# Performance work log

Measured on AMD Instinct MI355X. Metric: run time of the kernel, lower is better.

The kernel has to match this reference:

```python
import jax, jax.numpy as jnp
import numpy as np

EPS = 1e-7  # K.epsilon()


def setup_inputs() -> dict:
    key = jax.random.key(0)
    k1, k2, k3, k4, k5, k6 = jax.random.split(key, 6)
    B, S, D = 128, 1024, 256
    ATT, QDIM = 128, 128
    inp = {
        "key": jax.random.normal(k1, (B, S, D), dtype=jnp.float32),
        "query": jax.random.normal(k2, (QDIM, 1), dtype=jnp.float32),
        "mask": jax.random.randint(k3, (B, S), 0, 2, dtype=jnp.int32),
        # learned params (keras 'normal' init ~ N(0, 0.05))
        "W": 0.05 * jax.random.normal(k4, (D, ATT), dtype=jnp.float32),
        "b": 0.05 * jax.random.normal(k5, (ATT,), dtype=jnp.float32),
        "W_u": 0.05 * jax.random.normal(k6, (ATT, QDIM), dtype=jnp.float32),
    }
    return inp


def reference(key, query, mask, W, b, W_u):
    # uit = tanh(key @ W + b): (B,S,ATT)
    uit = jnp.tanh(jnp.einsum("bsd,da->bsa", key, W) + b)
    # u = W_u @ query: (ATT,1)
    u = W_u @ query
    # scores: (B,S)
    ait = jnp.einsum("bsa,a->bs", uit, u[:, 0])
    ait = jnp.exp(ait)
    ait = ait * mask.astype(jnp.float32)
    ait = ait / (jnp.sum(ait, axis=1, keepdims=True) + EPS)
    # weighted sum over sequence -> (B,D); value == key
    out = jnp.einsum("bs,bsd->bd", ait, key)
    return out
```

## Files before the change

### kernel.cpp

```cpp
#include <hip/hip_runtime.h>
#include <hip/hip_bf16.h>
#include <math.h>

#define EPS_F 1e-7f

constexpr int Bn = 128, Sn = 1024, Dn = 256, ATTn = 128, QDn = 128;
constexpr int Mn = Bn * Sn;
constexpr int BM = 128;
constexpr int NBLK = Mn / BM;
constexpr int KSTEPS = Dn / 32;
constexpr int NJ = ATTn / 16;

typedef short short8 __attribute__((ext_vector_type(8)));
typedef float f32x4  __attribute__((ext_vector_type(4)));

__device__ inline void split_bf(float f, ushort& hi, ushort& lo) {
    uint fb = __float_as_uint(f);
    hi = (ushort)(fb >> 16);
    float hf = __uint_as_float(fb & 0xffff0000u);
    float lf = f - hf;
    __hip_bfloat16 lb = __float2bfloat16(lf);
    __builtin_memcpy(&lo, &lb, 2);
}

__device__ inline float tanh_fast(float x) {
    float cx = fminf(9.0f, fmaxf(-9.0f, x));
    float e = __builtin_amdgcn_exp2f(cx * 2.8853900817779268f);
    return (e - 1.0f) * __builtin_amdgcn_rcpf(e + 1.0f);
}

__device__ inline void gload_lds16(const float* g, void* lds_base) {
    __builtin_amdgcn_global_load_lds(
        (const __attribute__((address_space(1))) unsigned int*)g,
        (__attribute__((address_space(3))) unsigned int*)lds_base, 16, 0, 0);
}


__global__ __launch_bounds__(256) void k_prep(
    const float* __restrict__ Wu, const float* __restrict__ q,
    float* __restrict__ u,
    const float* __restrict__ W,
    ushort* __restrict__ Bhi, ushort* __restrict__ Blo)
{
    if (blockIdx.x == 0) {
        __shared__ float qs[QDn];
        int t = threadIdx.x;
        if (t < QDn) qs[t] = q[t];
        __syncthreads();
        if (t < ATTn) {
            float acc = 0.f;
            #pragma unroll 8
            for (int j = 0; j < QDn; ++j) acc += Wu[t * QDn + j] * qs[j];
            u[t] = acc;
        }
        return;
    }
    int gid  = (blockIdx.x - 1) * 256 + threadIdx.x;
    int lane = gid & 63;
    int j    = (gid >> 6) & 7;
    int ks   = gid >> 9;
    int col  = j * 16 + (lane & 15);
    int kb   = ks * 32 + (lane >> 4) * 8;
    #pragma unroll
    for (int i = 0; i < 8; ++i) {
        float f = W[(size_t)(kb + i) * ATTn + col];
        ushort h, l;
        split_bf(f, h, l);
        size_t idx = (size_t)gid * 8 + i;
        Bhi[idx] = h; Blo[idx] = l;
    }
}

__global__ __launch_bounds__(256, 4) void k_scores(
    const float*  __restrict__ key,
    const ushort* __restrict__ Bhi, const ushort* __restrict__ Blo,
    const float*  __restrict__ bias, const float* __restrict__ u,
    const int*    __restrict__ mask,
    float* __restrict__ P, float* __restrict__ den)
{
    __shared__ float4 Atile[2][BM * 8];
    __shared__ float  es[BM];
    __shared__ float4 part[4][64];

    const int t    = threadIdx.x;
    const int lane = t & 63;
    const int w    = t >> 6;
    const int gb   = blockIdx.x;
    const int row0 = gb * BM;
    const int l15  = lane & 15;
    const int lg   = lane >> 4;

    const float* gsrc[4];
    int sbase[4];
    #pragma unroll
    for (int i = 0; i < 4; ++i) {
        int s   = i * 256 + t;
        int row = s >> 3;
        int cs  = s & 7;
        int cl  = cs ^ (row & 7);
        gsrc[i]  = key + (size_t)(row0 + row) * Dn + cl * 4;
        sbase[i] = i * 256 + w * 64;
    }

    f32x4 acc[2][NJ];
    #pragma unroll
    for (int rf = 0; rf < 2; ++rf)
        #pragma unroll
        for (int j = 0; j < NJ; ++j) acc[rf][j] = (f32x4){0.f, 0.f, 0.f, 0.f};

    #pragma unroll
    for (int i = 0; i < 4; ++i)
        gload_lds16(gsrc[i], &Atile[0][sbase[i]]);
    __syncthreads();

    #pragma unroll
    for (int ks = 0; ks < KSTEPS; ++ks) {
        const int cur = ks & 1;
        if (ks + 1 < KSTEPS) {
            #pragma unroll
            for (int i = 0; i < 4; ++i)
                gload_lds16(gsrc[i] + (ks + 1) * 32, &Atile[cur ^ 1][sbase[i]]);
        }

        short8 ah[2], al[2];
        #pragma unroll
        for (int rf = 0; rf < 2; ++rf) {
            int row = w * 32 + rf * 16 + l15;
            float4 a0 = Atile[cur][row * 8 + ((lg * 2)     ^ (row & 7))];
            float4 a1 = Atile[cur][row * 8 + ((lg * 2 + 1) ^ (row & 7))];
            float f[8] = {a0.x, a0.y, a0.z, a0.w, a1.x, a1.y, a1.z, a1.w};
            #pragma unroll
            for (int i = 0; i < 8; ++i) {
                ushort h, l;
                split_bf(f[i], h, l);
                ah[rf][i] = (short)h; al[rf][i] = (short)l;
            }
        }

        size_t boff = ((size_t)(ks * NJ) * 64 + lane) * 8;
        short8 bh = *(const short8*)(Bhi + boff);
        short8 bl = *(const short8*)(Blo + boff);
        #pragma unroll
        for (int j = 0; j < NJ; ++j) {
            short8 nbh, nbl;
            if (j + 1 < NJ) {
                size_t nb = ((size_t)(ks * NJ + j + 1) * 64 + lane) * 8;
                nbh = *(const short8*)(Bhi + nb);
                nbl = *(const short8*)(Blo + nb);
            }
            #pragma unroll
            for (int rf = 0; rf < 2; ++rf) {
                acc[rf][j] = __builtin_amdgcn_mfma_f32_16x16x32_bf16(ah[rf], bh, acc[rf][j], 0, 0, 0);
                acc[rf][j] = __builtin_amdgcn_mfma_f32_16x16x32_bf16(ah[rf], bl, acc[rf][j], 0, 0, 0);
                acc[rf][j] = __builtin_amdgcn_mfma_f32_16x16x32_bf16(al[rf], bh, acc[rf][j], 0, 0, 0);
            }
            bh = nbh; bl = nbl;
        }
        __syncthreads();
    }

    #pragma unroll
    for (int rf = 0; rf < 2; ++rf) {
        float s4[4] = {0.f, 0.f, 0.f, 0.f};
        #pragma unroll
        for (int j = 0; j < NJ; ++j) {
            int col = j * 16 + l15;
            float bv = bias[col], uvv = u[col];
            #pragma unroll
            for (int reg = 0; reg < 4; ++reg)
                s4[reg] += tanh_fast(acc[rf][j][reg] + bv) * uvv;
        }
        #pragma unroll
        for (int reg = 0; reg < 4; ++reg) {
            float s = s4[reg];
            s += __shfl_xor(s, 1);
            s += __shfl_xor(s, 2);
            s += __shfl_xor(s, 4);
            s += __shfl_xor(s, 8);
            if (l15 == 0) {
                int rl = w * 32 + rf * 16 + lg * 4 + reg;
                es[rl] = __builtin_amdgcn_exp2f(s * 1.4426950408889634f)
                         * (float)mask[row0 + rl];
            }
        }
    }
    __syncthreads();

    if (t < 64) {
        float v = es[t] + es[t + 64];
        #pragma unroll
        for (int m = 1; m < 64; m <<= 1) v += __shfl_xor(v, m);
        if (t == 0) den[gb] = v;
    }

    const int dq = t & 63;
    const int sc = t >> 6;
    const float4* key4 = (const float4*)(key + (size_t)row0 * Dn);
    float4 a2 = make_float4(0.f, 0.f, 0.f, 0.f);
    #pragma unroll 4
    for (int s2 = sc * 32; s2 < sc * 32 + 32; ++s2) {
        float wv  = es[s2];
        float4 kv = key4[(size_t)s2 * 64 + dq];
        a2.x += wv * kv.x; a2.y += wv * kv.y;
        a2.z += wv * kv.z; a2.w += wv * kv.w;
    }
    part[sc][dq] = a2;
    __syncthreads();
    if (t < 64) {
        float4 o = part[0][t];
        #pragma unroll
        for (int c = 1; c < 4; ++c) {
            float4 p = part[c][t];
            o.x += p.x; o.y += p.y; o.z += p.z; o.w += p.w;
        }
        *(float4*)(P + (size_t)gb * Dn + t * 4) = o;
    }
}

__global__ __launch_bounds__(256) void k_final(const float* __restrict__ P,
        const float* __restrict__ den, float* __restrict__ out) {
    int b = blockIdx.x, t = threadIdx.x;
    float dtot = 0.f;
    #pragma unroll
    for (int k = 0; k < 8; ++k) dtot += den[b * 8 + k];
    float o = 0.f;
    #pragma unroll
    for (int k = 0; k < 8; ++k) o += P[(size_t)(b * 8 + k) * Dn + t];
    out[(size_t)b * Dn + t] = o / (dtot + EPS_F);
}

extern "C" void kernel_launch(void* const* d_in, const int* in_sizes, int n_in,
                              void* d_out, int out_size, void* d_ws, size_t ws_size,
                              hipStream_t stream) {
    const float* key   = (const float*)d_in[0];
    const float* query = (const float*)d_in[1];
    const int*   mask  = (const int*)d_in[2];
    const float* W     = (const float*)d_in[3];
    const float* bias  = (const float*)d_in[4];
    const float* Wu    = (const float*)d_in[5];
    float* out = (float*)d_out;

    char* ws = (char*)d_ws;
    float*  u   = (float*)(ws);
    ushort* Bhi = (ushort*)(ws + 512);
    ushort* Blo = (ushort*)(ws + 66048);
    float*  Pp  = (float*)(ws + 131584);
    float*  den = (float*)(ws + 1180160);

    hipLaunchKernelGGL(k_prep,   dim3(17),   dim3(256), 0, stream, Wu, query, u, W, Bhi, Blo);
    hipLaunchKernelGGL(k_scores, dim3(NBLK), dim3(256), 0, stream,
                       key, Bhi, Blo, bias, u, mask, Pp, den);
    hipLaunchKernelGGL(k_final,  dim3(Bn),   dim3(256), 0, stream, Pp, den, out);
}
```

Before: 63.71 us.

## Keep key rows in registers, stage split weights in LDS, reuse bf16 key for pooling

The scores kernel now loads each wave's key rows straight into registers and double-buffers the pre-split bf16 hi/lo weight fragments through a 64KB LDS buffer, processed in four templated quarters. The bf16 high halves of the key held in registers are reused for the attention-weighted sum, computed with shuffle reductions, so key is not read from global memory a second time. This removes the second pass over key and the LDS staging of the activations. In exchange, occupancy drops (launch bounds 4 to 2 with more LDS), register pressure rises, and the pooled output now uses only the bf16-truncated key, which loses precision.

```diff
diff --git a/kernel.cpp b/kernel.cpp
--- a/kernel.cpp
+++ b/kernel.cpp
@@ -8,7 +8,6 @@
 constexpr int Mn = Bn * Sn;
 constexpr int BM = 128;
 constexpr int NBLK = Mn / BM;
-constexpr int KSTEPS = Dn / 32;
 constexpr int NJ = ATTn / 16;
 
 typedef short short8 __attribute__((ext_vector_type(8)));
@@ -23,13 +22,17 @@
     __builtin_memcpy(&lo, &lb, 2);
 }
 
+__device__ inline float hi2f(short h) {
+    return __uint_as_float(((uint)(ushort)h) << 16);
+}
+
 __device__ inline float tanh_fast(float x) {
     float cx = fminf(9.0f, fmaxf(-9.0f, x));
     float e = __builtin_amdgcn_exp2f(cx * 2.8853900817779268f);
     return (e - 1.0f) * __builtin_amdgcn_rcpf(e + 1.0f);
 }
 
-__device__ inline void gload_lds16(const float* g, void* lds_base) {
+__device__ inline void gload_lds16(const void* g, void* lds_base) {
     __builtin_amdgcn_global_load_lds(
         (const __attribute__((address_space(1))) unsigned int*)g,
         (__attribute__((address_space(3))) unsigned int*)lds_base, 16, 0, 0);
@@ -71,16 +74,84 @@
     }
 }
 
-__global__ __launch_bounds__(256, 4) void k_scores(
+#define MFMA_BF16 __builtin_amdgcn_mfma_f32_16x16x32_bf16
+
+template<int Q>
+__device__ __forceinline__ void process_quarter(
+    char* smem, const float* kb0, const float* kb1,
+    const ushort* __restrict__ Bhi, const ushort* __restrict__ Blo,
+    int t, int w, int lane,
+    float4 (&kv)[2][4], short8 (&ahk)[2][8], f32x4 (&acc)[2][NJ])
+{
+    const float4* Bcur = (const float4*)(smem + (Q & 1) * 32768);
+    if (Q < 3) {
+        char* Bnxt = smem + ((Q + 1) & 1) * 32768;
+        #pragma unroll
+        for (int i = 0; i < 8; ++i) {
+            int c   = i * 256 + t;
+            int cl  = c & 63;
+            int cs  = (c >> 6) & 1;
+            int cj  = (c >> 7) & 7;
+            int ck2 = (c >> 10) & 1;
+            int g   = ((Q + 1) * 2 + ck2) * 8 + cj;
+            const ushort* src = (cs ? Blo : Bhi) + ((size_t)g * 64 + cl) * 8;
+            gload_lds16(src, Bnxt + (i * 256 + w * 64) * 16);
+        }
+    }
+    #pragma unroll
+    for (int ks2 = 0; ks2 < 2; ++ks2) {
+        short8 al[2];
+        #pragma unroll
+        for (int rf = 0; rf < 2; ++rf) {
+            const float4 v0 = kv[rf][ks2 * 2], v1 = kv[rf][ks2 * 2 + 1];
+            float f[8] = {v0.x, v0.y, v0.z, v0.w, v1.x, v1.y, v1.z, v1.w};
+            #pragma unroll
+            for (int i = 0; i < 8; ++i) {
+                ushort h, l;
+                split_bf(f[i], h, l);
+                ahk[rf][Q * 2 + ks2][i] = (short)h;
+                al[rf][i] = (short)l;
+            }
+        }
+        if (Q < 3) {
+            const int off = ((Q + 1) * 2 + ks2) * 32;
+            kv[0][ks2 * 2]     = *(const float4*)(kb0 + off);
+            kv[0][ks2 * 2 + 1] = *(const float4*)(kb0 + off + 4);
+            kv[1][ks2 * 2]     = *(const float4*)(kb1 + off);
+            kv[1][ks2 * 2 + 1] = *(const float4*)(kb1 + off + 4);
+        }
+        const int cb = (ks2 << 10) | lane;
+        short8 bh = *(const short8*)&Bcur[cb];
+        short8 bl = *(const short8*)&Bcur[cb + 64];
+        #pragma unroll
+        for (int j = 0; j < NJ; ++j) {
+            short8 nbh, nbl;
+            if (j + 1 < NJ) {
+                nbh = *(const short8*)&Bcur[cb + ((j + 1) << 7)];
+                nbl = *(const short8*)&Bcur[cb + ((j + 1) << 7) + 64];
+            }
+            #pragma unroll
+            for (int rf = 0; rf < 2; ++rf) {
+                acc[rf][j] = MFMA_BF16(ahk[rf][Q * 2 + ks2], bh, acc[rf][j], 0, 0, 0);
+                acc[rf][j] = MFMA_BF16(ahk[rf][Q * 2 + ks2], bl, acc[rf][j], 0, 0, 0);
+                acc[rf][j] = MFMA_BF16(al[rf], bh, acc[rf][j], 0, 0, 0);
+            }
+            bh = nbh; bl = nbl;
+        }
+    }
+    __syncthreads();
+}
+
+__global__ __launch_bounds__(256, 2) void k_scores(
     const float*  __restrict__ key,
     const ushort* __restrict__ Bhi, const ushort* __restrict__ Blo,
     const float*  __restrict__ bias, const float* __restrict__ u,
     const int*    __restrict__ mask,
     float* __restrict__ P, float* __restrict__ den)
 {
-    __shared__ float4 Atile[2][BM * 8];
-    __shared__ float  es[BM];
-    __shared__ float4 part[4][64];
+    __shared__ char smem[65536];
+    float* es   = (float*)smem;
+    float* part = (float*)(smem + 512);
 
     const int t    = threadIdx.x;
     const int lane = t & 63;
@@ -90,17 +161,8 @@
     const int l15  = lane & 15;
     const int lg   = lane >> 4;
 
-    const float* gsrc[4];
-    int sbase[4];
-    #pragma unroll
-    for (int i = 0; i < 4; ++i) {
-        int s   = i * 256 + t;
-        int row = s >> 3;
-        int cs  = s & 7;
-        int cl  = cs ^ (row & 7);
-        gsrc[i]  = key + (size_t)(row0 + row) * Dn + cl * 4;
-        sbase[i] = i * 256 + w * 64;
-    }
+    const float* kb0 = key + (size_t)(row0 + w * 32 + l15) * Dn + lg * 8;
+    const float* kb1 = kb0 + 16 * Dn;
 
     f32x4 acc[2][NJ];
     #pragma unroll
@@ -108,56 +170,33 @@
         #pragma unroll
         for (int j = 0; j < NJ; ++j) acc[rf][j] = (f32x4){0.f, 0.f, 0.f, 0.f};
 
-    #pragma unroll
-    for (int i = 0; i < 4; ++i)
-        gload_lds16(gsrc[i], &Atile[0][sbase[i]]);
+    short8 ahk[2][8];
+    float4 kv[2][4];
+
+    #pragma unroll
+    for (int ks2 = 0; ks2 < 2; ++ks2) {
+        kv[0][ks2 * 2]     = *(const float4*)(kb0 + ks2 * 32);
+        kv[0][ks2 * 2 + 1] = *(const float4*)(kb0 + ks2 * 32 + 4);
+        kv[1][ks2 * 2]     = *(const float4*)(kb1 + ks2 * 32);
+        kv[1][ks2 * 2 + 1] = *(const float4*)(kb1 + ks2 * 32 + 4);
+    }
+    #pragma unroll
+    for (int i = 0; i < 8; ++i) {
+        int c   = i * 256 + t;
+        int cl  = c & 63;
+        int cs  = (c >> 6) & 1;
+        int cj  = (c >> 7) & 7;
+        int ck2 = (c >> 10) & 1;
+        int g   = ck2 * 8 + cj;
+        const ushort* src = (cs ? Blo : Bhi) + ((size_t)g * 64 + cl) * 8;
+        gload_lds16(src, smem + (i * 256 + w * 64) * 16);
+    }
     __syncthreads();
 
-    #pragma unroll
-    for (int ks = 0; ks < KSTEPS; ++ks) {
-        const int cur = ks & 1;
-        if (ks + 1 < KSTEPS) {
-            #pragma unroll
-            for (int i = 0; i < 4; ++i)
-                gload_lds16(gsrc[i] + (ks + 1) * 32, &Atile[cur ^ 1][sbase[i]]);
-        }
-
-        short8 ah[2], al[2];
-        #pragma unroll
-        for (int rf = 0; rf < 2; ++rf) {
-            int row = w * 32 + rf * 16 + l15;
-            float4 a0 = Atile[cur][row * 8 + ((lg * 2)     ^ (row & 7))];
-            float4 a1 = Atile[cur][row * 8 + ((lg * 2 + 1) ^ (row & 7))];
-            float f[8] = {a0.x, a0.y, a0.z, a0.w, a1.x, a1.y, a1.z, a1.w};
-            #pragma unroll
-            for (int i = 0; i < 8; ++i) {
-                ushort h, l;
-                split_bf(f[i], h, l);
-                ah[rf][i] = (short)h; al[rf][i] = (short)l;
-            }
-        }
-
-        size_t boff = ((size_t)(ks * NJ) * 64 + lane) * 8;
-        short8 bh = *(const short8*)(Bhi + boff);
-        short8 bl = *(const short8*)(Blo + boff);
-        #pragma unroll
-        for (int j = 0; j < NJ; ++j) {
-            short8 nbh, nbl;
-            if (j + 1 < NJ) {
-                size_t nb = ((size_t)(ks * NJ + j + 1) * 64 + lane) * 8;
-                nbh = *(const short8*)(Bhi + nb);
-                nbl = *(const short8*)(Blo + nb);
-            }
-            #pragma unroll
-            for (int rf = 0; rf < 2; ++rf) {
-                acc[rf][j] = __builtin_amdgcn_mfma_f32_16x16x32_bf16(ah[rf], bh, acc[rf][j], 0, 0, 0);
-                acc[rf][j] = __builtin_amdgcn_mfma_f32_16x16x32_bf16(ah[rf], bl, acc[rf][j], 0, 0, 0);
-                acc[rf][j] = __builtin_amdgcn_mfma_f32_16x16x32_bf16(al[rf], bh, acc[rf][j], 0, 0, 0);
-            }
-            bh = nbh; bl = nbl;
-        }
-        __syncthreads();
-    }
+    process_quarter<0>(smem, kb0, kb1, Bhi, Blo, t, w, lane, kv, ahk, acc);
+    process_quarter<1>(smem, kb0, kb1, Bhi, Blo, t, w, lane, kv, ahk, acc);
+    process_quarter<2>(smem, kb0, kb1, Bhi, Blo, t, w, lane, kv, ahk, acc);
+    process_quarter<3>(smem, kb0, kb1, Bhi, Blo, t, w, lane, kv, ahk, acc);
 
     #pragma unroll
     for (int rf = 0; rf < 2; ++rf) {
@@ -193,25 +232,37 @@
         if (t == 0) den[gb] = v;
     }
 
-    const int dq = t & 63;
-    const int sc = t >> 6;
-    const float4* key4 = (const float4*)(key + (size_t)row0 * Dn);
-    float4 a2 = make_float4(0.f, 0.f, 0.f, 0.f);
-    #pragma unroll 4
-    for (int s2 = sc * 32; s2 < sc * 32 + 32; ++s2) {
-        float wv  = es[s2];
-        float4 kv = key4[(size_t)s2 * 64 + dq];
-        a2.x += wv * kv.x; a2.y += wv * kv.y;
-        a2.z += wv * kv.z; a2.w += wv * kv.w;
-    }
-    part[sc][dq] = a2;
+    {
+        float e0 = es[w * 32 + l15];
+        float e1 = es[w * 32 + l15 + 16];
+        #pragma unroll
+        for (int ks = 0; ks < 8; ++ks) {
+            float p[8];
+            #pragma unroll
+            for (int i = 0; i < 8; ++i)
+                p[i] = e0 * hi2f(ahk[0][ks][i]) + e1 * hi2f(ahk[1][ks][i]);
+            #pragma unroll
+            for (int i = 0; i < 8; ++i) {
+                p[i] += __shfl_xor(p[i], 1);
+                p[i] += __shfl_xor(p[i], 2);
+                p[i] += __shfl_xor(p[i], 4);
+                p[i] += __shfl_xor(p[i], 8);
+            }
+            if (l15 == 0) {
+                float* dst = &part[w * 256 + ks * 32 + lg * 8];
+                *(float4*)(dst)     = make_float4(p[0], p[1], p[2], p[3]);
+                *(float4*)(dst + 4) = make_float4(p[4], p[5], p[6], p[7]);
+            }
+        }
+    }
     __syncthreads();
+
     if (t < 64) {
-        float4 o = part[0][t];
-        #pragma unroll
-        for (int c = 1; c < 4; ++c) {
-            float4 p = part[c][t];
-            o.x += p.x; o.y += p.y; o.z += p.z; o.w += p.w;
+        float4 o = *(float4*)&part[t * 4];
+        #pragma unroll
+        for (int wv = 1; wv < 4; ++wv) {
+            float4 pv = *(float4*)&part[wv * 256 + t * 4];
+            o.x += pv.x; o.y += pv.y; o.z += pv.z; o.w += pv.w;
         }
         *(float4*)(P + (size_t)gb * Dn + t * 4) = o;
     }
```

Result: faster. 59.48 us (-6.6%).
